# Optimization experiments

Measured on AMD Instinct MI355X. Metric: run time of the kernel, lower is better.

Reference implementation:

```python
import jax, jax.numpy as jnp
import numpy as np

D, DFF, H, NLAYERS, B, L, U = 1536, 2048, 8, 2, 16, 64, 64
EPS = 1e-5


def _ln(x, w, b):
    mu = jnp.mean(x, axis=-1, keepdims=True)
    var = jnp.mean((x - mu) ** 2, axis=-1, keepdims=True)
    return (x - mu) / jnp.sqrt(var + EPS) * w + b


def _mha(q_in, kv_in, qkv_w, qkv_b, out_w, out_b, mask):
    # torch nn.MultiheadAttention: packed in_proj [3D,D], out_proj [D,D]
    d = q_in.shape[-1]
    hd = d // H
    wq, wk, wv = jnp.split(qkv_w, 3, axis=0)
    bq, bk, bv = jnp.split(qkv_b, 3, axis=0)
    q = q_in @ wq.T + bq
    k = kv_in @ wk.T + bk
    v = kv_in @ wv.T + bv
    def heads(t):
        b_, s_, _ = t.shape
        return t.reshape(b_, s_, H, hd).transpose(0, 2, 1, 3)  # [B,H,S,hd]
    q, k, v = heads(q), heads(k), heads(v)
    scores = jnp.einsum('bhqd,bhkd->bhqk', q, k) / jnp.sqrt(jnp.float32(hd))
    if mask is not None:
        scores = scores + mask  # [Sq,Sk] broadcast
    attn = jax.nn.softmax(scores, axis=-1)
    o = jnp.einsum('bhqk,bhkd->bhqd', attn, v)
    b_, _, s_, _ = o.shape
    o = o.transpose(0, 2, 1, 3).reshape(b_, s_, d)
    return o @ out_w.T + out_b


def setup_inputs() -> dict:
    key = jax.random.key(0)
    ks = jax.random.split(key, 16)
    f = lambda k, shp: (jax.random.normal(k, shp, jnp.float32) * 0.02)
    Lyr = NLAYERS
    return {
        'x': jax.random.normal(ks[0], (B, L, U, D), jnp.float32),
        'pooler_w': f(ks[1], (1, D)),
        'pooler_b': jnp.zeros((1,), jnp.float32),
        'pos_embed': f(ks[2], (1, 128, D)),
        'sa_qkv_w': f(ks[3], (Lyr, 3 * D, D)),
        'sa_qkv_b': jnp.zeros((Lyr, 3 * D), jnp.float32),
        'sa_out_w': f(ks[4], (Lyr, D, D)),
        'sa_out_b': jnp.zeros((Lyr, D), jnp.float32),
        'ca_qkv_w': f(ks[5], (Lyr, 3 * D, D)),
        'ca_qkv_b': jnp.zeros((Lyr, 3 * D), jnp.float32),
        'ca_out_w': f(ks[6], (Lyr, D, D)),
        'ca_out_b': jnp.zeros((Lyr, D), jnp.float32),
        'ff1_w': f(ks[7], (Lyr, DFF, D)),
        'ff1_b': jnp.zeros((Lyr, DFF), jnp.float32),
        'ff2_w': f(ks[8], (Lyr, D, DFF)),
        'ff2_b': jnp.zeros((Lyr, D), jnp.float32),
        'ln1_w': jnp.ones((Lyr, D), jnp.float32),
        'ln1_b': jnp.zeros((Lyr, D), jnp.float32),
        'ln2_w': jnp.ones((Lyr, D), jnp.float32),
        'ln2_b': jnp.zeros((Lyr, D), jnp.float32),
        'ln3_w': jnp.ones((Lyr, D), jnp.float32),
        'ln3_b': jnp.zeros((Lyr, D), jnp.float32),
    }


def reference(x, pooler_w, pooler_b, pos_embed,
              sa_qkv_w, sa_qkv_b, sa_out_w, sa_out_b,
              ca_qkv_w, ca_qkv_b, ca_out_w, ca_out_b,
              ff1_w, ff1_b, ff2_w, ff2_b,
              ln1_w, ln1_b, ln2_w, ln2_b, ln3_w, ln3_b):
    b, l, u, d = x.shape
    # SelfAttentionPooling over utterance tokens (vectorized over dialogue dim)
    logits = jnp.einsum('blud,d->blu', x, pooler_w[0]) + pooler_b[0]
    att = jax.nn.softmax(logits, axis=-1)
    pooled = jnp.einsum('blu,blud->bld', att, x)

    pos = pos_embed[:, :l, :]
    memory = pooled + pos
    tgt = pooled + pos
    causal = jnp.triu(jnp.full((l, l), -jnp.inf, jnp.float32), 1)

    h = tgt
    for i in range(NLAYERS):
        # post-norm TransformerDecoderLayer (torch default norm_first=False)
        h = _ln(h + _mha(h, h, sa_qkv_w[i], sa_qkv_b[i], sa_out_w[i], sa_out_b[i], causal),
                ln1_w[i], ln1_b[i])
        h = _ln(h + _mha(h, memory, ca_qkv_w[i], ca_qkv_b[i], ca_out_w[i], ca_out_b[i], None),
                ln2_w[i], ln2_b[i])
        ff = jax.nn.relu(h @ ff1_w[i].T + ff1_b[i]) @ ff2_w[i].T + ff2_b[i]
        h = _ln(h + ff, ln3_w[i], ln3_b[i])

    # loop over prefixes t=1..L-1 taking the last position == causal positions 0..L-2
    return h[:, : l - 1, :]
```

## Files before the change

kernel.cpp:

```cpp
#include <hip/hip_runtime.h>
#include <math.h>

#define D_MODEL 1536
#define NH      8
#define HD      192
#define BB      16
#define LL      64
#define UU      64
#define NTOK    1024
#define EPSF    1e-5f

typedef __bf16 bf16;
typedef __bf16 bf16x4_t __attribute__((ext_vector_type(4)));
typedef __bf16 bf16x8_t __attribute__((ext_vector_type(8)));
typedef float  f32x4_t  __attribute__((ext_vector_type(4)));

__device__ __forceinline__ void gload_lds16(const bf16* g, bf16* l) {
    __builtin_amdgcn_global_load_lds((const __attribute__((address_space(1))) void*)g,
                                     (__attribute__((address_space(3))) void*)l, 16, 0, 0);
}

__global__ __launch_bounds__(256)
void prep_kernel(const float* __restrict__ x, const float* __restrict__ pw,
                 const float* __restrict__ pb, const float* __restrict__ pos,
                 float* __restrict__ h, bf16* __restrict__ hb,
                 bf16* __restrict__ memb,
                 const float* __restrict__ s0, const float* __restrict__ s1,
                 const float* __restrict__ s2, const float* __restrict__ s3,
                 const float* __restrict__ s4, const float* __restrict__ s5,
                 bf16* __restrict__ dst)
{
    const int t = threadIdx.x;
    if (blockIdx.x >= 1024) {
        const int c0 = 3538944, c1 = 4718592, c2 = 8257536,
                  c3 = 9437184, c4 = 11010048, c5 = 12582912;
        for (int i = (blockIdx.x - 1024) * 256 + t; i < c5; i += 2048 * 256) {
            const float* s; int j;
            if      (i < c0) { s = s0; j = i; }
            else if (i < c1) { s = s1; j = i - c0; }
            else if (i < c2) { s = s2; j = i - c1; }
            else if (i < c3) { s = s3; j = i - c2; }
            else if (i < c4) { s = s4; j = i - c3; }
            else             { s = s5; j = i - c4; }
            const float4 v = ((const float4*)s)[j];
            bf16x4_t o = { (bf16)v.x, (bf16)v.y, (bf16)v.z, (bf16)v.w };
            ((bf16x4_t*)dst)[i] = o;
        }
        return;
    }
    __shared__ float red[2][4];
    const int wave = t >> 6, lane = t & 63;
    const int bl = blockIdx.x, l = bl & (LL - 1);
    const float* xb = x + (size_t)bl * UU * D_MODEL;

    float pwr[6];
#pragma unroll
    for (int j = 0; j < 6; ++j) pwr[j] = pw[t + j * 256];
    const float pb0 = pb[0];

    float xv[2][6];
#pragma unroll
    for (int j = 0; j < 6; ++j) xv[0][j] = xb[t + j * 256];

    float m = -__builtin_inff(), den = 0.f;
    float acc[6] = {0.f, 0.f, 0.f, 0.f, 0.f, 0.f};

    for (int u = 0; u < UU; ++u) {
        const int cur = u & 1;
        if (u < UU - 1) {
            const float* xn = xb + (size_t)(u + 1) * D_MODEL;
#pragma unroll
            for (int j = 0; j < 6; ++j) xv[cur ^ 1][j] = xn[t + j * 256];
        }
        float p = 0.f;
#pragma unroll
        for (int j = 0; j < 6; ++j) p += xv[cur][j] * pwr[j];
#pragma unroll
        for (int off = 32; off; off >>= 1) p += __shfl_xor(p, off, 64);
        if (lane == 0) red[cur][wave] = p;
        __syncthreads();
        const float logit = red[cur][0] + red[cur][1] + red[cur][2] + red[cur][3] + pb0;
        const float nm = fmaxf(m, logit);
        const float sc = __expf(m - nm);
        const float w  = __expf(logit - nm);
#pragma unroll
        for (int j = 0; j < 6; ++j) acc[j] = acc[j] * sc + w * xv[cur][j];
        den = den * sc + w;
        m = nm;
    }

    const float inv = 1.f / den;
    const size_t db = (size_t)bl * D_MODEL;
    const int pp = l * D_MODEL;
#pragma unroll
    for (int j = 0; j < 6; ++j) {
        const int d = t + j * 256;
        const float v = acc[j] * inv + pos[pp + d];
        h[db + d] = v;
        hb[db + d] = (bf16)v;
        memb[db + d] = (bf16)v;
    }
}

template<int MODE, bool DUAL, int SPLITK>
__global__ __launch_bounds__(512, 6)
void gemm8_kernel(const bf16* __restrict__ A, const bf16* __restrict__ W,
                  const float* __restrict__ bias, void* __restrict__ Cv,
                  int N, int K, int split,
                  const bf16* __restrict__ A2, const bf16* __restrict__ W2,
                  const float* __restrict__ bias2, void* __restrict__ Cv2, int N2)
{
    __shared__ bf16 As[2][64 * 64];
    __shared__ bf16 Bs[2][128 * 64];
    const int t = threadIdx.x, wave = t >> 6, lane = t & 63;

    const int T = gridDim.x, fid = blockIdx.x;
    int vid = (fid & 7) * (T >> 3) + (fid >> 3);
    const bf16* Ap = A; const bf16* Wp = W; const float* bp = bias;
    void* Cp = Cv; int Nn = N;
    if (DUAL && vid >= split) { vid -= split; Ap = A2; Wp = W2; bp = bias2; Cp = Cv2; Nn = N2; }
    int kslice = 0;
    if (SPLITK == 2) { kslice = vid & 1; vid >>= 1; }
    else if (SPLITK == 4) { kslice = vid & 3; vid >>= 2; }
    const int m0 = (vid & 15) * 64;
    const int n0 = (vid >> 4) * 128;
    const int Kl = SPLITK ? K / SPLITK : K;
    const int kbase = kslice * Kl;

    const int wm = wave >> 2, wn = wave & 3;
    const int frow = lane & 15, kq = lane >> 4, s = frow & 7;
    const int lr = lane >> 3;
    const int g8 = ((lane & 7) ^ lr) * 8;

    f32x4_t acc[2][2] = {};

    const bf16* Abase = Ap + (size_t)(m0 + wave * 8 + lr) * K + kbase + g8;
    const bf16* Wbase = Wp + (size_t)(n0 + wave * 8 + lr) * K + kbase + g8;

    auto STAGE = [&](int buf, int tile) {
        const int k0 = tile << 6;
        gload_lds16(Abase + k0, &As[buf][wave * 512]);
        gload_lds16(Wbase + k0, &Bs[buf][wave * 512]);
        gload_lds16(Wbase + k0 + (size_t)64 * K, &Bs[buf][4096 + wave * 512]);
    };
    auto COMPUTE = [&](int buf) {
#pragma unroll
        for (int kk = 0; kk < 2; ++kk) {
            const int gg = (((kk << 2) | kq) ^ s) * 8;
            bf16x8_t af[2], bv[2];
#pragma unroll
            for (int mi = 0; mi < 2; ++mi)
                af[mi] = *(const bf16x8_t*)&As[buf][(wm * 32 + mi * 16 + frow) * 64 + gg];
#pragma unroll
            for (int ni = 0; ni < 2; ++ni)
                bv[ni] = *(const bf16x8_t*)&Bs[buf][(wn * 32 + ni * 16 + frow) * 64 + gg];
#pragma unroll
            for (int mi = 0; mi < 2; ++mi)
#pragma unroll
                for (int ni = 0; ni < 2; ++ni)
                    acc[mi][ni] = __builtin_amdgcn_mfma_f32_16x16x32_bf16(af[mi], bv[ni], acc[mi][ni], 0, 0, 0);
        }
    };

    const int nt = Kl >> 6;
    STAGE(0, 0);
    STAGE(1, 1);
    for (int tt = 0; tt + 1 < nt; ++tt) {
        asm volatile("s_waitcnt vmcnt(3)" ::: "memory");
        __builtin_amdgcn_s_barrier();
        COMPUTE(tt & 1);
        __builtin_amdgcn_s_barrier();
        if (tt + 2 < nt) STAGE(tt & 1, tt + 2);
    }
    asm volatile("s_waitcnt vmcnt(0)" ::: "memory");
    __builtin_amdgcn_s_barrier();
    COMPUTE((nt - 1) & 1);

    float* Cpart = (float*)Cp + (SPLITK ? (size_t)kslice * NTOK * Nn : 0);
    const int crow = m0 + wm * 32 + kq * 4;
    const int ccol = n0 + wn * 32 + frow;
#pragma unroll
    for (int mi = 0; mi < 2; ++mi)
#pragma unroll
        for (int ni = 0; ni < 2; ++ni) {
            const int col = ccol + ni * 16;
            const float bvv = (SPLITK && kslice) ? 0.f : bp[col];
            const int rb = crow + mi * 16;
#pragma unroll
            for (int j = 0; j < 4; ++j) {
                float v = acc[mi][ni][j] + bvv;
                if (MODE == 0) {
                    Cpart[(size_t)(rb + j) * Nn + col] = v;
                } else if (MODE == 1) {
                    ((bf16*)Cp)[(size_t)(rb + j) * Nn + col] = (bf16)fmaxf(v, 0.f);
                } else {
                    ((bf16*)Cp)[(size_t)(rb + j) * Nn + col] = (bf16)v;
                }
            }
        }
}

__global__ __launch_bounds__(256)
void reduce_relu_kernel(const float* __restrict__ p0, const float* __restrict__ p1,
                        bf16* __restrict__ dst, int n4)
{
    const int i = blockIdx.x * 256 + threadIdx.x;
    if (i >= n4) return;
    const float4 a = ((const float4*)p0)[i];
    const float4 b = ((const float4*)p1)[i];
    bf16x4_t o = { (bf16)fmaxf(a.x + b.x, 0.f), (bf16)fmaxf(a.y + b.y, 0.f),
                   (bf16)fmaxf(a.z + b.z, 0.f), (bf16)fmaxf(a.w + b.w, 0.f) };
    ((bf16x4_t*)dst)[i] = o;
}

template<bool CAUSAL, bool Q4>
__global__ __launch_bounds__(256)
void attn_kernel(const bf16* __restrict__ qb, const float* __restrict__ qp, int PN,
                 int qstride, int qoff0,
                 const bf16* __restrict__ kbuf, int kstride, int koff0,
                 const bf16* __restrict__ vbuf, int vstride, int voff0,
                 bf16* __restrict__ out)
{
    __shared__ float kv[HD * 64];
    __shared__ float sc[16 * 64];
    const int t = threadIdx.x, wave = t >> 6, lane = t & 63;
    const int bh = blockIdx.x >> 2, qh = blockIdx.x & 3;
    const int b = bh >> 3, hh = bh & 7;
    const int t0 = b * 64;
    const float scale = rsqrtf((float)HD);

    for (int i = 0; i < 48; ++i) {
        const int idx = t + i * 256;
        const int r = idx / HD, c = idx % HD;
        kv[c * 64 + (r ^ (c & 31))] =
            (float)kbuf[(size_t)(t0 + r) * kstride + koff0 + hh * HD + c];
    }
    __syncthreads();

    for (int qi = 0; qi < 4; ++qi) {
        const int ql = wave * 4 + qi;
        const int q = qh * 16 + ql;
        const size_t qb0 = (size_t)(t0 + q) * qstride + qoff0 + hh * HD;
        float a = 0.f;
#pragma unroll 8
        for (int d = 0; d < HD; ++d) {
            float qv;
            if (Q4) qv = qp[qb0 + d] + qp[(size_t)PN + qb0 + d]
                       + qp[2 * (size_t)PN + qb0 + d] + qp[3 * (size_t)PN + qb0 + d];
            else    qv = (float)qb[qb0 + d];
            a += qv * kv[d * 64 + (lane ^ (d & 31))];
        }
        a *= scale;
        if (CAUSAL && lane > q) a = -__builtin_inff();
        float m = a;
#pragma unroll
        for (int off = 32; off; off >>= 1) m = fmaxf(m, __shfl_xor(m, off, 64));
        float e = (CAUSAL && lane > q) ? 0.f : __expf(a - m);
        float s = e;
#pragma unroll
        for (int off = 32; off; off >>= 1) s += __shfl_xor(s, off, 64);
        sc[ql * 64 + lane] = e / s;
    }
    __syncthreads();

    for (int i = 0; i < 48; ++i) {
        const int idx = t + i * 256;
        const int r = idx / HD, c = idx % HD;
        kv[r * HD + c] = (float)vbuf[(size_t)(t0 + r) * vstride + voff0 + hh * HD + c];
    }
    __syncthreads();

    for (int qi = 0; qi < 4; ++qi) {
        const int ql = wave * 4 + qi;
        const int q = qh * 16 + ql;
        float o0 = 0.f, o1 = 0.f, o2 = 0.f;
#pragma unroll 8
        for (int k = 0; k < 64; ++k) {
            const float p = sc[ql * 64 + k];
            o0 += p * kv[k * HD + lane];
            o1 += p * kv[k * HD + 64 + lane];
            o2 += p * kv[k * HD + 128 + lane];
        }
        bf16* op = out + (size_t)(t0 + q) * D_MODEL + hh * HD;
        op[lane] = (bf16)o0; op[64 + lane] = (bf16)o1; op[128 + lane] = (bf16)o2;
    }
}

template<bool SLICE>
__global__ __launch_bounds__(256)
void ln_kernel(const float* __restrict__ a, const float* __restrict__ p, int PN,
               const float* __restrict__ w, const float* __restrict__ bb,
               float* __restrict__ out, bf16* __restrict__ outb,
               float* __restrict__ out2)
{
    __shared__ float red[8];
    const int tok = blockIdx.x, t = threadIdx.x;
    const int wave = t >> 6, lane = t & 63;
    const float* ap = a + (size_t)tok * D_MODEL;
    const float* pp = p + (size_t)tok * D_MODEL;
    float v[6];
    float s = 0.f;
#pragma unroll
    for (int j = 0; j < 6; ++j) {
        const int d = t + j * 256;
        v[j] = ap[d] + pp[d] + pp[(size_t)PN + d]
             + pp[2 * (size_t)PN + d] + pp[3 * (size_t)PN + d];
        s += v[j];
    }
#pragma unroll
    for (int off = 32; off; off >>= 1) s += __shfl_xor(s, off, 64);
    if (lane == 0) red[wave] = s;
    __syncthreads();
    const float mu = (red[0] + red[1] + red[2] + red[3]) * (1.f / D_MODEL);
    float s2 = 0.f;
#pragma unroll
    for (int j = 0; j < 6; ++j) { const float d = v[j] - mu; s2 += d * d; }
#pragma unroll
    for (int off = 32; off; off >>= 1) s2 += __shfl_xor(s2, off, 64);
    if (lane == 0) red[4 + wave] = s2;
    __syncthreads();
    const float var = (red[4] + red[5] + red[6] + red[7]) * (1.f / D_MODEL);
    const float inv = rsqrtf(var + EPSF);
    const int bq = tok >> 6, lq = tok & 63;
#pragma unroll
    for (int j = 0; j < 6; ++j) {
        const int d = t + j * 256;
        const float o = (v[j] - mu) * inv * w[d] + bb[d];
        out[(size_t)tok * D_MODEL + d] = o;
        outb[(size_t)tok * D_MODEL + d] = (bf16)o;
        if (SLICE && lq < 63) out2[(size_t)(bq * 63 + lq) * D_MODEL + d] = o;
    }
}

extern "C" void kernel_launch(void* const* d_in, const int* in_sizes, int n_in,
                              void* d_out, int out_size, void* d_ws, size_t ws_size,
                              hipStream_t stream)
{
    (void)in_sizes; (void)n_in; (void)out_size; (void)ws_size;
    const float* x        = (const float*)d_in[0];
    const float* pooler_w = (const float*)d_in[1];
    const float* pooler_b = (const float*)d_in[2];
    const float* pos      = (const float*)d_in[3];
    const float* sa_qkv_w = (const float*)d_in[4];
    const float* sa_qkv_b = (const float*)d_in[5];
    const float* sa_out_w = (const float*)d_in[6];
    const float* sa_out_b = (const float*)d_in[7];
    const float* ca_qkv_w = (const float*)d_in[8];
    const float* ca_qkv_b = (const float*)d_in[9];
    const float* ca_out_w = (const float*)d_in[10];
    const float* ca_out_b = (const float*)d_in[11];
    const float* ff1_w    = (const float*)d_in[12];
    const float* ff1_b    = (const float*)d_in[13];
    const float* ff2_w    = (const float*)d_in[14];
    const float* ff2_b    = (const float*)d_in[15];
    const float* ln1_w    = (const float*)d_in[16];
    const float* ln1_b    = (const float*)d_in[17];
    const float* ln2_w    = (const float*)d_in[18];
    const float* ln2_b    = (const float*)d_in[19];
    const float* ln3_w    = (const float*)d_in[20];
    const float* ln3_b    = (const float*)d_in[21];
    float* outp = (float*)d_out;

    char* ws = (char*)d_ws;
    size_t off = 0;
    auto alloc = [&](size_t bytes) { char* p = ws + off; off += (bytes + 255) & ~(size_t)255; return p; };

    const size_t E_QKV = (size_t)4608 * D_MODEL;
    const size_t E_SQ  = (size_t)D_MODEL * D_MODEL;
    const size_t E_F1  = (size_t)2048 * D_MODEL;
    const int    PN    = NTOK * D_MODEL;

    bf16* wb_sa_qkv = (bf16*)alloc(2 * E_QKV * 2);
    bf16* wb_sa_out = (bf16*)alloc(2 * E_SQ * 2);
    bf16* wb_ca_qkv = (bf16*)alloc(2 * E_QKV * 2);
    bf16* wb_ca_out = (bf16*)alloc(2 * E_SQ * 2);
    bf16* wb_ff1    = (bf16*)alloc(2 * E_F1 * 2);
    bf16* wb_ff2    = (bf16*)alloc(2 * E_F1 * 2);
    float* h     = (float*)alloc((size_t)NTOK * D_MODEL * 4);
    bf16*  hb    = (bf16*) alloc((size_t)NTOK * D_MODEL * 2);
    bf16*  memb  = (bf16*) alloc((size_t)NTOK * D_MODEL * 2);
    bf16*  qkvb  = (bf16*) alloc((size_t)NTOK * 4608 * 2);
    float* cq4   = (float*)alloc((size_t)PN * 4 * 4);
    bf16*  ckv0  = (bf16*) alloc((size_t)NTOK * 3072 * 2);
    bf16*  ckv1  = (bf16*) alloc((size_t)NTOK * 3072 * 2);
    bf16*  attno = (bf16*) alloc((size_t)NTOK * D_MODEL * 2);
    float* proj4 = (float*)alloc((size_t)PN * 4 * 4);
    float* f1p01 = (float*)alloc((size_t)NTOK * 2048 * 4 * 2);
    bf16*  ffmid = (bf16*) alloc((size_t)NTOK * 2048 * 2);

    float* f1p1 = f1p01 + (size_t)NTOK * 2048;

    prep_kernel<<<3072, 256, 0, stream>>>(x, pooler_w, pooler_b, pos, h, hb, memb,
                                          sa_qkv_w, sa_out_w, ca_qkv_w,
                                          ca_out_w, ff1_w, ff2_w, wb_sa_qkv);

    gemm8_kernel<2, true, 0><<<768, 512, 0, stream>>>(
        memb, wb_ca_qkv + (size_t)1536 * D_MODEL, ca_qkv_b + 1536,
        ckv0, 3072, D_MODEL, 384,
        memb, wb_ca_qkv + E_QKV + (size_t)1536 * D_MODEL, ca_qkv_b + 4608 + 1536,
        ckv1, 3072);

    for (int i = 0; i < 2; ++i) {
        bf16* ckv = i ? ckv1 : ckv0;

        gemm8_kernel<2, false, 0><<<16 * 36, 512, 0, stream>>>(
            hb, wb_sa_qkv + (size_t)i * E_QKV, sa_qkv_b + (size_t)i * 4608,
            qkvb, 4608, D_MODEL, 0, nullptr, nullptr, nullptr, nullptr, 0);
        attn_kernel<true, false><<<BB * NH * 4, 256, 0, stream>>>(
            qkvb, nullptr, 0, 4608, 0, qkvb, 4608, 1536, qkvb, 4608, 3072, attno);
        gemm8_kernel<0, false, 4><<<16 * 12 * 4, 512, 0, stream>>>(
            attno, wb_sa_out + (size_t)i * E_SQ, sa_out_b + (size_t)i * D_MODEL,
            proj4, D_MODEL, D_MODEL, 0, nullptr, nullptr, nullptr, nullptr, 0);
        ln_kernel<false><<<NTOK, 256, 0, stream>>>(
            h, proj4, PN, ln1_w + i * D_MODEL, ln1_b + i * D_MODEL, h, hb, nullptr);

        gemm8_kernel<0, false, 4><<<16 * 12 * 4, 512, 0, stream>>>(
            hb, wb_ca_qkv + (size_t)i * E_QKV, ca_qkv_b + (size_t)i * 4608,
            cq4, D_MODEL, D_MODEL, 0, nullptr, nullptr, nullptr, nullptr, 0);
        attn_kernel<false, true><<<BB * NH * 4, 256, 0, stream>>>(
            nullptr, cq4, PN, 1536, 0, ckv, 3072, 0, ckv, 3072, 1536, attno);
        gemm8_kernel<0, false, 4><<<16 * 12 * 4, 512, 0, stream>>>(
            attno, wb_ca_out + (size_t)i * E_SQ, ca_out_b + (size_t)i * D_MODEL,
            proj4, D_MODEL, D_MODEL, 0, nullptr, nullptr, nullptr, nullptr, 0);
        ln_kernel<false><<<NTOK, 256, 0, stream>>>(
            h, proj4, PN, ln2_w + i * D_MODEL, ln2_b + i * D_MODEL, h, hb, nullptr);

        gemm8_kernel<0, false, 2><<<16 * 16 * 2, 512, 0, stream>>>(
            hb, wb_ff1 + (size_t)i * E_F1, ff1_b + (size_t)i * 2048,
            f1p01, 2048, D_MODEL, 0, nullptr, nullptr, nullptr, nullptr, 0);
        reduce_relu_kernel<<<2048, 256, 0, stream>>>(
            f1p01, f1p1, ffmid, NTOK * 2048 / 4);
        gemm8_kernel<0, false, 4><<<16 * 12 * 4, 512, 0, stream>>>(
            ffmid, wb_ff2 + (size_t)i * E_F1, ff2_b + (size_t)i * D_MODEL,
            proj4, D_MODEL, 2048, 0, nullptr, nullptr, nullptr, nullptr, 0);
        if (i == 0)
            ln_kernel<false><<<NTOK, 256, 0, stream>>>(
                h, proj4, PN, ln3_w, ln3_b, h, hb, nullptr);
        else
            ln_kernel<true><<<NTOK, 256, 0, stream>>>(
                h, proj4, PN, ln3_w + D_MODEL, ln3_b + D_MODEL, h, hb, outp);
    }
}
```

Baseline: 686.2 us.

## Fuse split-K reduce+ReLU into FF2 GEMM A-load and use split-K 2

Removes the separate reduce_relu kernel by having a new FF2 GEMM read both fp32 FF1 partials, sum them, apply ReLU and convert to bf16 while staging the A tile into LDS. All split-K-4 GEMMs (attention out-projections, cross-attention Q, FF2) become split-K 2, which halves the fp32 partial traffic read by the LayerNorm and attention kernels but also halves the grid size. The fused A load goes through registers instead of direct global-to-LDS loads, which may expose more latency in the FF2 loop.

```diff
diff --git a/kernel.cpp b/kernel.cpp
--- a/kernel.cpp
+++ b/kernel.cpp
@@ -121,7 +121,6 @@
     if (DUAL && vid >= split) { vid -= split; Ap = A2; Wp = W2; bp = bias2; Cp = Cv2; Nn = N2; }
     int kslice = 0;
     if (SPLITK == 2) { kslice = vid & 1; vid >>= 1; }
-    else if (SPLITK == 4) { kslice = vid & 3; vid >>= 2; }
     const int m0 = (vid & 15) * 64;
     const int n0 = (vid >> 4) * 128;
     const int Kl = SPLITK ? K / SPLITK : K;
@@ -200,20 +199,101 @@
         }
 }
 
-__global__ __launch_bounds__(256)
-void reduce_relu_kernel(const float* __restrict__ p0, const float* __restrict__ p1,
-                        bf16* __restrict__ dst, int n4)
+__global__ __launch_bounds__(512, 4)
+void gemm_ff2_kernel(const float* __restrict__ p0, const float* __restrict__ p1,
+                     const float* __restrict__ bias, float* __restrict__ C,
+                     const bf16* __restrict__ W, int N, int K)
 {
-    const int i = blockIdx.x * 256 + threadIdx.x;
-    if (i >= n4) return;
-    const float4 a = ((const float4*)p0)[i];
-    const float4 b = ((const float4*)p1)[i];
-    bf16x4_t o = { (bf16)fmaxf(a.x + b.x, 0.f), (bf16)fmaxf(a.y + b.y, 0.f),
-                   (bf16)fmaxf(a.z + b.z, 0.f), (bf16)fmaxf(a.w + b.w, 0.f) };
-    ((bf16x4_t*)dst)[i] = o;
-}
-
-template<bool CAUSAL, bool Q4>
+    __shared__ bf16 As[2][64 * 64];
+    __shared__ bf16 Bs[2][128 * 64];
+    const int t = threadIdx.x, wave = t >> 6, lane = t & 63;
+
+    const int T = gridDim.x, fid = blockIdx.x;
+    int vid = (fid & 7) * (T >> 3) + (fid >> 3);
+    const int kslice = vid & 1; vid >>= 1;
+    const int m0 = (vid & 15) * 64;
+    const int n0 = (vid >> 4) * 128;
+    const int Kl = K >> 1;
+    const int kbase = kslice * Kl;
+
+    const int wm = wave >> 2, wn = wave & 3;
+    const int frow = lane & 15, kq = lane >> 4, s = frow & 7;
+    const int lr = lane >> 3;
+    const int g8 = ((lane & 7) ^ lr) * 8;
+
+    f32x4_t acc[2][2] = {};
+
+    const int arow = m0 + wave * 8 + lr;
+    const float* P0 = p0 + (size_t)arow * K + kbase + g8;
+    const float* P1 = p1 + (size_t)arow * K + kbase + g8;
+    const bf16* Wbase = W + (size_t)(n0 + wave * 8 + lr) * K + kbase + g8;
+
+    auto STAGE = [&](int buf, int tile) {
+        const int k0 = tile << 6;
+        const f32x4_t a0 = *(const f32x4_t*)(P0 + k0);
+        const f32x4_t a1 = *(const f32x4_t*)(P0 + k0 + 4);
+        const f32x4_t b0 = *(const f32x4_t*)(P1 + k0);
+        const f32x4_t b1 = *(const f32x4_t*)(P1 + k0 + 4);
+        bf16x8_t av;
+#pragma unroll
+        for (int j = 0; j < 4; ++j) {
+            av[j]     = (bf16)fmaxf(a0[j] + b0[j], 0.f);
+            av[4 + j] = (bf16)fmaxf(a1[j] + b1[j], 0.f);
+        }
+        *(bf16x8_t*)&As[buf][wave * 512 + lane * 8] = av;
+        gload_lds16(Wbase + k0, &Bs[buf][wave * 512]);
+        gload_lds16(Wbase + k0 + (size_t)64 * K, &Bs[buf][4096 + wave * 512]);
+    };
+    auto COMPUTE = [&](int buf) {
+#pragma unroll
+        for (int kk = 0; kk < 2; ++kk) {
+            const int gg = (((kk << 2) | kq) ^ s) * 8;
+            bf16x8_t af[2], bv[2];
+#pragma unroll
+            for (int mi = 0; mi < 2; ++mi)
+                af[mi] = *(const bf16x8_t*)&As[buf][(wm * 32 + mi * 16 + frow) * 64 + gg];
+#pragma unroll
+            for (int ni = 0; ni < 2; ++ni)
+                bv[ni] = *(const bf16x8_t*)&Bs[buf][(wn * 32 + ni * 16 + frow) * 64 + gg];
+#pragma unroll
+            for (int mi = 0; mi < 2; ++mi)
+#pragma unroll
+                for (int ni = 0; ni < 2; ++ni)
+                    acc[mi][ni] = __builtin_amdgcn_mfma_f32_16x16x32_bf16(af[mi], bv[ni], acc[mi][ni], 0, 0, 0);
+        }
+    };
+
+    const int nt = Kl >> 6;
+    STAGE(0, 0);
+    STAGE(1, 1);
+    for (int tt = 0; tt + 1 < nt; ++tt) {
+        asm volatile("s_waitcnt vmcnt(2) lgkmcnt(0)" ::: "memory");
+        __builtin_amdgcn_s_barrier();
+        COMPUTE(tt & 1);
+        __builtin_amdgcn_s_barrier();
+        if (tt + 2 < nt) STAGE(tt & 1, tt + 2);
+    }
+    asm volatile("s_waitcnt vmcnt(0) lgkmcnt(0)" ::: "memory");
+    __builtin_amdgcn_s_barrier();
+    COMPUTE((nt - 1) & 1);
+
+    float* Cpart = C + (size_t)kslice * NTOK * N;
+    const int crow = m0 + wm * 32 + kq * 4;
+    const int ccol = n0 + wn * 32 + frow;
+#pragma unroll
+    for (int mi = 0; mi < 2; ++mi)
+#pragma unroll
+        for (int ni = 0; ni < 2; ++ni) {
+            const int col = ccol + ni * 16;
+            const float bvv = kslice ? 0.f : bias[col];
+            const int rb = crow + mi * 16;
+#pragma unroll
+            for (int j = 0; j < 4; ++j)
+                Cpart[(size_t)(rb + j) * N + col] = acc[mi][ni][j] + bvv;
+        }
+}
+
+template<bool CAUSAL, bool Q2>
 __global__ __launch_bounds__(256)
 void attn_kernel(const bf16* __restrict__ qb, const float* __restrict__ qp, int PN,
                  int qstride, int qoff0,
@@ -245,8 +325,7 @@
 #pragma unroll 8
         for (int d = 0; d < HD; ++d) {
             float qv;
-            if (Q4) qv = qp[qb0 + d] + qp[(size_t)PN + qb0 + d]
-                       + qp[2 * (size_t)PN + qb0 + d] + qp[3 * (size_t)PN + qb0 + d];
+            if (Q2) qv = qp[qb0 + d] + qp[(size_t)PN + qb0 + d];
             else    qv = (float)qb[qb0 + d];
             a += qv * kv[d * 64 + (lane ^ (d & 31))];
         }
@@ -288,7 +367,8 @@
 
 template<bool SLICE>
 __global__ __launch_bounds__(256)
-void ln_kernel(const float* __restrict__ a, const float* __restrict__ p, int PN,
+void ln_kernel(const float* __restrict__ a, const float* __restrict__ r,
+               const float* __restrict__ r2,
                const float* __restrict__ w, const float* __restrict__ bb,
                float* __restrict__ out, bf16* __restrict__ outb,
                float* __restrict__ out2)
@@ -297,14 +377,14 @@
     const int tok = blockIdx.x, t = threadIdx.x;
     const int wave = t >> 6, lane = t & 63;
     const float* ap = a + (size_t)tok * D_MODEL;
-    const float* pp = p + (size_t)tok * D_MODEL;
+    const float* rp = r + (size_t)tok * D_MODEL;
+    const float* rp2 = r2 + (size_t)tok * D_MODEL;
     float v[6];
     float s = 0.f;
 #pragma unroll
     for (int j = 0; j < 6; ++j) {
         const int d = t + j * 256;
-        v[j] = ap[d] + pp[d] + pp[(size_t)PN + d]
-             + pp[2 * (size_t)PN + d] + pp[3 * (size_t)PN + d];
+        v[j] = ap[d] + rp[d] + rp2[d];
         s += v[j];
     }
 #pragma unroll
@@ -380,23 +460,24 @@
     bf16*  hb    = (bf16*) alloc((size_t)NTOK * D_MODEL * 2);
     bf16*  memb  = (bf16*) alloc((size_t)NTOK * D_MODEL * 2);
     bf16*  qkvb  = (bf16*) alloc((size_t)NTOK * 4608 * 2);
-    float* cq4   = (float*)alloc((size_t)PN * 4 * 4);
+    float* cq01  = (float*)alloc((size_t)PN * 4 * 2);
     bf16*  ckv0  = (bf16*) alloc((size_t)NTOK * 3072 * 2);
     bf16*  ckv1  = (bf16*) alloc((size_t)NTOK * 3072 * 2);
     bf16*  attno = (bf16*) alloc((size_t)NTOK * D_MODEL * 2);
-    float* proj4 = (float*)alloc((size_t)PN * 4 * 4);
+    float* proj01= (float*)alloc((size_t)PN * 4 * 2);
     float* f1p01 = (float*)alloc((size_t)NTOK * 2048 * 4 * 2);
-    bf16*  ffmid = (bf16*) alloc((size_t)NTOK * 2048 * 2);
-
-    float* f1p1 = f1p01 + (size_t)NTOK * 2048;
+
+    float* cq1   = cq01   + (size_t)PN;
+    float* proj1 = proj01 + (size_t)PN;
+    float* f1p1  = f1p01  + (size_t)NTOK * 2048;
 
     prep_kernel<<<3072, 256, 0, stream>>>(x, pooler_w, pooler_b, pos, h, hb, memb,
                                           sa_qkv_w, sa_out_w, ca_qkv_w,
                                           ca_out_w, ff1_w, ff2_w, wb_sa_qkv);
 
-    gemm8_kernel<2, true, 0><<<768, 512, 0, stream>>>(
+    gemm8_kernel<2, true, 0><<<16 * 24 * 2, 512, 0, stream>>>(
         memb, wb_ca_qkv + (size_t)1536 * D_MODEL, ca_qkv_b + 1536,
-        ckv0, 3072, D_MODEL, 384,
+        ckv0, 3072, D_MODEL, 16 * 24,
         memb, wb_ca_qkv + E_QKV + (size_t)1536 * D_MODEL, ca_qkv_b + 4608 + 1536,
         ckv1, 3072);
 
@@ -408,36 +489,34 @@
             qkvb, 4608, D_MODEL, 0, nullptr, nullptr, nullptr, nullptr, 0);
         attn_kernel<true, false><<<BB * NH * 4, 256, 0, stream>>>(
             qkvb, nullptr, 0, 4608, 0, qkvb, 4608, 1536, qkvb, 4608, 3072, attno);
-        gemm8_kernel<0, false, 4><<<16 * 12 * 4, 512, 0, stream>>>(
+        gemm8_kernel<0, false, 2><<<16 * 12 * 2, 512, 0, stream>>>(
             attno, wb_sa_out + (size_t)i * E_SQ, sa_out_b + (size_t)i * D_MODEL,
-            proj4, D_MODEL, D_MODEL, 0, nullptr, nullptr, nullptr, nullptr, 0);
+            proj01, D_MODEL, D_MODEL, 0, nullptr, nullptr, nullptr, nullptr, 0);
         ln_kernel<false><<<NTOK, 256, 0, stream>>>(
-            h, proj4, PN, ln1_w + i * D_MODEL, ln1_b + i * D_MODEL, h, hb, nullptr);
-
-        gemm8_kernel<0, false, 4><<<16 * 12 * 4, 512, 0, stream>>>(
+            h, proj01, proj1, ln1_w + i * D_MODEL, ln1_b + i * D_MODEL, h, hb, nullptr);
+
+        gemm8_kernel<0, false, 2><<<16 * 12 * 2, 512, 0, stream>>>(
             hb, wb_ca_qkv + (size_t)i * E_QKV, ca_qkv_b + (size_t)i * 4608,
-            cq4, D_MODEL, D_MODEL, 0, nullptr, nullptr, nullptr, nullptr, 0);
+            cq01, D_MODEL, D_MODEL, 0, nullptr, nullptr, nullptr, nullptr, 0);
         attn_kernel<false, true><<<BB * NH * 4, 256, 0, stream>>>(
-            nullptr, cq4, PN, 1536, 0, ckv, 3072, 0, ckv, 3072, 1536, attno);
-        gemm8_kernel<0, false, 4><<<16 * 12 * 4, 512, 0, stream>>>(
+            nullptr, cq01, PN, 1536, 0, ckv, 3072, 0, ckv, 3072, 1536, attno);
+        gemm8_kernel<0, false, 2><<<16 * 12 * 2, 512, 0, stream>>>(
             attno, wb_ca_out + (size_t)i * E_SQ, ca_out_b + (size_t)i * D_MODEL,
-            proj4, D_MODEL, D_MODEL, 0, nullptr, nullptr, nullptr, nullptr, 0);
+            proj01, D_MODEL, D_MODEL, 0, nullptr, nullptr, nullptr, nullptr, 0);
         ln_kernel<false><<<NTOK, 256, 0, stream>>>(
-            h, proj4, PN, ln2_w + i * D_MODEL, ln2_b + i * D_MODEL, h, hb, nullptr);
+            h, proj01, proj1, ln2_w + i * D_MODEL, ln2_b + i * D_MODEL, h, hb, nullptr);
 
         gemm8_kernel<0, false, 2><<<16 * 16 * 2, 512, 0, stream>>>(
             hb, wb_ff1 + (size_t)i * E_F1, ff1_b + (size_t)i * 2048,
             f1p01, 2048, D_MODEL, 0, nullptr, nullptr, nullptr, nullptr, 0);
-        reduce_relu_kernel<<<2048, 256, 0, stream>>>(
-            f1p01, f1p1, ffmid, NTOK * 2048 / 4);
-        gemm8_kernel<0, false, 4><<<16 * 12 * 4, 512, 0, stream>>>(
-            ffmid, wb_ff2 + (size_t)i * E_F1, ff2_b + (size_t)i * D_MODEL,
-            proj4, D_MODEL, 2048, 0, nullptr, nullptr, nullptr, nullptr, 0);
+        gemm_ff2_kernel<<<16 * 12 * 2, 512, 0, stream>>>(
+            f1p01, f1p1, ff2_b + (size_t)i * D_MODEL, proj01,
+            wb_ff2 + (size_t)i * E_F1, D_MODEL, 2048);
         if (i == 0)
             ln_kernel<false><<<NTOK, 256, 0, stream>>>(
-                h, proj4, PN, ln3_w, ln3_b, h, hb, nullptr);
+                h, proj01, proj1, ln3_w, ln3_b, h, hb, nullptr);
         else
             ln_kernel<true><<<NTOK, 256, 0, stream>>>(
-                h, proj4, PN, ln3_w + D_MODEL, ln3_b + D_MODEL, h, hb, outp);
-    }
-}
+                h, proj01, proj1, ln3_w + D_MODEL, ln3_b + D_MODEL, h, hb, outp);
+    }
+}
```

Result: no change. 676.5 us (-1.4%).
